# Optimization experiments

Hardware: AMD Instinct MI355X
Metric: run time of the kernel (lower is better)

Reference implementation:

```python
import jax, jax.numpy as jnp
import numpy as np

N_SP, N_SPAT = 20000, 10000
E_SS, E_BIP, E_SP = 160000, 320000, 320000
H, C = 4, 64  # GAT heads / per-head channels (hidden_channels=64, concat=False)
EPS = 1e-6


def _gat(xs, xd, row, col, ea, Ws, Wd, a_s, a_d, a_e, We, b, num_dst, heads, ch, self_loops, concat):
    # PyG GATConv with edge_dim: linear -> per-head additive attention -> softmax over incoming edges -> scatter-add
    hs = (xs @ Ws).reshape(-1, heads, ch)          # [Ns,H,C]
    hd = (xd @ Wd).reshape(-1, heads, ch)          # [Nd,H,C]
    al_s = jnp.sum(hs * a_s, -1)                   # [Ns,H]
    al_d = jnp.sum(hd * a_d, -1)                   # [Nd,H]
    if self_loops:
        # add_self_loops with fill_value='mean': loop edge_attr = mean of incoming edge_attr per node
        cnt = jax.ops.segment_sum(jnp.ones((row.shape[0],), ea.dtype), col, num_dst)
        loop_ea = jax.ops.segment_sum(ea, col, num_dst) / jnp.maximum(cnt, 1.0)[:, None]
        loops = jnp.arange(num_dst, dtype=row.dtype)
        row = jnp.concatenate([row, loops])
        col = jnp.concatenate([col, loops])
        ea = jnp.concatenate([ea, loop_ea], 0)
    he = (ea @ We).reshape(-1, heads, ch)          # [E,H,C]
    al = jax.nn.leaky_relu(al_s[row] + al_d[col] + jnp.sum(he * a_e, -1), 0.2)  # [E,H]
    m = jax.ops.segment_max(al, col, num_segments=num_dst)
    ex = jnp.exp(al - m[col])
    den = jax.ops.segment_sum(ex, col, num_segments=num_dst)
    alpha = ex / (den[col] + 1e-16)
    out = jax.ops.segment_sum(hs[row] * alpha[..., None], col, num_segments=num_dst)  # [Nd,H,C]
    out = out.reshape(num_dst, heads * ch) if concat else out.mean(1)
    return out + b


def setup_inputs() -> dict:
    key = jax.random.key(0)
    ks = iter(jax.random.split(key, 64))
    f = lambda shape: jax.random.normal(next(ks), shape, jnp.float32)
    w = lambda shape: f(shape) / np.sqrt(shape[0])
    inp = {}
    inp['species_x_mean'] = f((N_SP, 32))
    inp['species_x_std'] = jax.random.uniform(next(ks), (N_SP, 32), jnp.float32)
    inp['traits_nanmask'] = jax.random.bernoulli(next(ks), 0.4, (N_SP, 32))
    inp['species_x_gen'] = f((N_SP, 64))
    inp['species_x_phylo'] = f((N_SP, 128))
    inp['spatial_x'] = f((N_SPAT, 12))
    inp['spatial_global_data'] = f((N_SPAT, 4))
    ei = lambda e, ns, nd: jnp.stack([jax.random.randint(next(ks), (e,), 0, ns, jnp.int32),
                                      jax.random.randint(next(ks), (e,), 0, nd, jnp.int32)])
    inp['ss_edge_index'] = ei(E_SS, N_SPAT, N_SPAT)
    inp['ss_edge_attr'] = jax.random.uniform(next(ks), (E_SS, 1), jnp.float32)
    inp['bip_edge_index'] = ei(E_BIP, N_SPAT, N_SP)
    inp['bip_edge_attr'] = jax.random.uniform(next(ks), (E_BIP, 1), jnp.float32)
    inp['sp_edge_index'] = ei(E_SP, N_SP, N_SP)
    inp['sp_edge_attr'] = jax.random.uniform(next(ks), (E_SP, 1), jnp.float32)
    # GAT conv params: space_gnn (sg0, sg1), species_gnn (pg0, pg1)
    for nm, din in [('sg0', 16), ('sg1', 64), ('pg0', 128), ('pg1', 64)]:
        inp[nm + '_W'] = w((din, H * C))
        inp[nm + '_as'] = f((H, C)) * 0.1
        inp[nm + '_ad'] = f((H, C)) * 0.1
        inp[nm + '_ae'] = f((H, C)) * 0.1
        inp[nm + '_We'] = w((1, H * C))
        inp[nm + '_b'] = jnp.zeros((C,), jnp.float32)
    # bipartite GATConv: heads=1, concat=True, src dim=hidden=64, dst dim=in_gen+in_phylo=192
    inp['bp_Ws'] = w((64, 64))
    inp['bp_Wd'] = w((192, 64))
    inp['bp_as'] = f((1, 64)) * 0.1
    inp['bp_ad'] = f((1, 64)) * 0.1
    inp['bp_ae'] = f((1, 64)) * 0.1
    inp['bp_We'] = w((1, 64))
    inp['bp_b'] = jnp.zeros((64,), jnp.float32)
    inp['sl_W'] = w((288, 64))
    inp['sl_b'] = jnp.zeros((64,), jnp.float32)
    inp['fc_W'] = w((64, 64))
    inp['fc_b'] = jnp.zeros((64,), jnp.float32)
    return inp


def reference(species_x_mean, species_x_std, traits_nanmask, species_x_gen, species_x_phylo,
              spatial_x, spatial_global_data, ss_edge_index, ss_edge_attr, bip_edge_index,
              bip_edge_attr, sp_edge_index, sp_edge_attr,
              sg0_W, sg0_as, sg0_ad, sg0_ae, sg0_We, sg0_b,
              sg1_W, sg1_as, sg1_ad, sg1_ae, sg1_We, sg1_b,
              pg0_W, pg0_as, pg0_ad, pg0_ae, pg0_We, pg0_b,
              pg1_W, pg1_as, pg1_ad, pg1_ae, pg1_We, pg1_b,
              bp_Ws, bp_Wd, bp_as, bp_ad, bp_ae, bp_We, bp_b,
              sl_W, sl_b, fc_W, fc_b):
    # inference path: no trait masking -> visibility = observed mask
    vis = (~traits_nanmask).astype(jnp.float32)
    sp_in = jnp.concatenate([species_x_mean, species_x_std, vis, species_x_gen, species_x_phylo], 1)
    sp_in = jax.nn.relu(sp_in @ sl_W + sl_b)                      # [N_SP,64]
    # spatial GNN (2 GATConv layers, heads=4, concat=False, self loops)
    h = jnp.concatenate([spatial_x, spatial_global_data], 1)      # [N_SPAT,16]
    r, c = ss_edge_index[0], ss_edge_index[1]
    h = jax.nn.relu(_gat(h, h, r, c, ss_edge_attr, sg0_W, sg0_W, sg0_as, sg0_ad, sg0_ae, sg0_We, sg0_b, N_SPAT, H, C, True, False))
    h = jax.nn.relu(_gat(h, h, r, c, ss_edge_attr, sg1_W, sg1_W, sg1_as, sg1_ad, sg1_ae, sg1_We, sg1_b, N_SPAT, H, C, True, False))
    # bipartite spatial->species GATConv (heads=1, concat=True, no self loops)
    part = jnp.concatenate([species_x_gen, species_x_phylo], 1)   # [N_SP,192]
    br, bc = bip_edge_index[0], bip_edge_index[1]
    sts = jax.nn.relu(_gat(h, part, br, bc, bip_edge_attr, bp_Ws, bp_Wd, bp_as, bp_ad, bp_ae, bp_We, bp_b, N_SP, 1, 64, False, True))
    # species GNN (2 GATConv layers)
    x = jnp.concatenate([sts, sp_in], 1)                          # [N_SP,128]
    pr, pc = sp_edge_index[0], sp_edge_index[1]
    x = jax.nn.relu(_gat(x, x, pr, pc, sp_edge_attr, pg0_W, pg0_W, pg0_as, pg0_ad, pg0_ae, pg0_We, pg0_b, N_SP, H, C, True, False))
    x = jax.nn.relu(_gat(x, x, pr, pc, sp_edge_attr, pg1_W, pg1_W, pg1_as, pg1_ad, pg1_ae, pg1_We, pg1_b, N_SP, H, C, True, False))
    ms = x @ fc_W + fc_b                                          # [N_SP, 2*out]
    mean, log_std = jnp.split(ms, 2, axis=-1)
    std = jax.nn.softplus(log_std) + EPS
    return mean, std
```

## Files before the change

### kernel.cpp

```cpp
#include <hip/hip_runtime.h>
#include <hip/hip_bf16.h>

#define NSP   20000
#define NSPAT 10000
#define ESS   160000
#define EBIP  320000
#define ESP   320000

static inline int cdiv_host(long a, long b) { return (int)((a + b - 1) / b); }

__device__ __forceinline__ float wave_red_sum(float p) {
#pragma unroll
  for (int m = 32; m >= 1; m >>= 1) p += __shfl_xor(p, m, 64);
  return p;
}
__device__ __forceinline__ float bf2f(unsigned short u) {
  return __uint_as_float(((unsigned int)u) << 16);
}
__device__ __forceinline__ unsigned short f2bf(float f) {
  unsigned int u = __float_as_uint(f);
  unsigned int r = (u + 0x7FFF + ((u >> 16) & 1)) >> 16;
  return (unsigned short)r;
}

__global__ void count3_kernel(
    const int* c1, int E1, int* cp1, int* rnk1, int n1,
    const int* c2, int E2, int* cp2, int* rnk2, int n2,
    const int* c3, int E3, int* cp3, int* rnk3, int n3,
    const unsigned int* __restrict__ mask, int* __restrict__ flag) {
  int b = blockIdx.x, t = threadIdx.x;
  if (b == gridDim.x - 1) {
    if (t < 64) {
      unsigned int w0 = mask[t], w1 = mask[t + 64], w2 = mask[t + 128], w3 = mask[t + 192];
      bool ai = (w0 <= 1u) && (w1 <= 1u) && (w2 <= 1u) && (w3 <= 1u);
      auto okf = [](unsigned int w) { return w == 0u || w == 0x3f800000u; };
      bool af = okf(w0) && okf(w1) && okf(w2) && okf(w3);
      unsigned long long bi = __ballot(ai), bf = __ballot(af);
      if (t == 0) *flag = (bi == ~0ull) ? 0 : ((bf == ~0ull) ? 2 : 1);
    }
    return;
  }
  int i = b * 256 + t;
  int total = E1 + E2 + E3;
  if (i >= total) return;
  int p = (i >> 8) & 7;
  if (i < E1) {
    int d = c1[i]; rnk1[i] = atomicAdd(&cp1[p * n1 + d], 1);
  } else if (i < E1 + E2) {
    int j = i - E1;
    int d = c2[j]; rnk2[j] = atomicAdd(&cp2[p * n2 + d], 1);
  } else {
    int j = i - E1 - E2;
    int d = c3[j]; rnk3[j] = atomicAdd(&cp3[p * n3 + d], 1);
  }
}

__global__ void merge3_kernel(int* cp1, int* c1, int n1,
                              int* cp2, int* c2, int n2,
                              int* cp3, int* c3, int n3) {
  int i = blockIdx.x * blockDim.x + threadIdx.x;
  int total = n1 + n2 + n3;
  if (i >= total) return;
  int *cp, *c; int n, d;
  if (i < n1) { cp = cp1; c = c1; n = n1; d = i; }
  else if (i < n1 + n2) { cp = cp2; c = c2; n = n2; d = i - n1; }
  else { cp = cp3; c = c3; n = n3; d = i - n1 - n2; }
  int s = 0;
#pragma unroll
  for (int p = 0; p < 8; ++p) { int t = cp[p * n + d]; cp[p * n + d] = s; s += t; }
  c[d] = s;
}

__global__ __launch_bounds__(1024) void scan3_kernel(
    const int* cntA, int nA, int* ptrA,
    const int* cntB, int nB, int* ptrB,
    const int* cntC, int nC, int* ptrC) {
  const int* cnt; int n; int* ptr;
  if (blockIdx.x == 0) { cnt = cntA; n = nA; ptr = ptrA; }
  else if (blockIdx.x == 1) { cnt = cntB; n = nB; ptr = ptrB; }
  else { cnt = cntC; n = nC; ptr = ptrC; }
  __shared__ int part[1024];
  int t = threadIdx.x;
  int ch = (n + 1023) / 1024;
  int beg = t * ch, end = min(beg + ch, n);
  int s = 0;
  for (int i = beg; i < end; ++i) s += cnt[i];
  part[t] = s;
  __syncthreads();
  for (int off = 1; off < 1024; off <<= 1) {
    int v = (t >= off) ? part[t - off] : 0;
    __syncthreads();
    part[t] += v;
    __syncthreads();
  }
  int run = (t == 0) ? 0 : part[t - 1];
  for (int i = beg; i < end; ++i) { ptr[i] = run; run += cnt[i]; }
  if (t == 1023) ptr[n] = part[1023];
}

struct DoteArgs { const float* We[5]; const float* ae[5]; float* dotes; };
struct PrepArgs {
  const float* mean; const float* stdv; const void* mask; const int* flag;
  const float* sx; const float* sg; float* spc96; float* h0;
};

__global__ void scatter3x_kernel(
    const int* r1, const int* c1, const float* e1, int E1, const int* p1, const int* cp1, const int* k1, int n1, int* s1, float* a1,
    const int* r2, const int* c2, const float* e2, int E2, const int* p2, const int* cp2, const int* k2, int n2, int* s2, float* a2,
    const int* r3, const int* c3, const float* e3, int E3, const int* p3, const int* cp3, const int* k3, int n3, int* s3, float* a3,
    DoteArgs da, PrepArgs pa) {
  const int NB_SC = (ESS + EBIP + ESP + 255) / 256;
  int b = blockIdx.x, t = threadIdx.x;
  if (b < NB_SC) {
    int i = b * 256 + t;
    if (i >= E1 + E2 + E3) return;
    int p = (i >> 8) & 7;
    if (i < E1) {
      int d = c1[i];
      int pos = p1[d] + cp1[p * n1 + d] + k1[i];
      s1[pos] = r1[i]; a1[pos] = e1[i];
    } else if (i < E1 + E2) {
      int j = i - E1;
      int d = c2[j];
      int pos = p2[d] + cp2[p * n2 + d] + k2[j];
      s2[pos] = r2[j]; a2[pos] = e2[j];
    } else {
      int j = i - E1 - E2;
      int d = c3[j];
      int pos = p3[d] + cp3[p * n3 + d] + k3[j];
      s3[pos] = r3[j]; a3[pos] = e3[j];
    }
  } else if (b < NB_SC + 5) {
    int lb = b - NB_SC;
    int n = (lb == 2) ? 64 : 256;
    if (t < n) {
      float p = wave_red_sum(da.We[lb][t] * da.ae[lb][t]);
      if ((t & 63) == 0) da.dotes[lb * 4 + (t >> 6)] = p;
    }
  } else {
    const long totA = (long)NSP * 96;
    const long totB = (long)NSPAT * 16;
    long i = (long)(b - NB_SC - 5) * 256 + t;
    if (i >= totA + totB) return;
    int mode = *pa.flag;
    if (i < totA) {
      int n = (int)(i / 96), c = (int)(i % 96);
      float v;
      if (c < 32) v = pa.mean[(long)n * 32 + c];
      else if (c < 64) v = pa.stdv[(long)n * 32 + (c - 32)];
      else {
        long j = (long)n * 32 + (c - 64);
        int mv;
        if (mode == 0) mv = ((const int*)pa.mask)[j];
        else if (mode == 2) mv = (((const float*)pa.mask)[j] != 0.0f);
        else mv = (int)((const unsigned char*)pa.mask)[j];
        v = mv ? 0.f : 1.f;
      }
      pa.spc96[i] = v;
    } else {
      long k = i - totA;
      int n = (int)(k / 16), c = (int)(k % 16);
      pa.h0[k] = (c < 12) ? pa.sx[(long)n * 12 + c] : pa.sg[(long)n * 4 + (c - 12)];
    }
  }
}

struct XSrc { const float* p[5]; int w[5]; int n; };
struct PJob {
  XSrc xs; int M, K;
  const float* W; const float* bias; int mode;
  const float* a_s; const float* a_d;
  float* al_s; float* al_d;
  float* Y; float* Y2;
};
struct LeafArgs {
  const int* ss_ptr; const float* ss_cea; float* ss_lea;
  const int* pp_ptr; const float* pp_cea; float* pp_lea;
};

__device__ __forceinline__ void proj64_body(const PJob& J, int bid,
                                            float* wl, float* xl) {
  constexpr int KC = 32;
  constexpr int BR = 32;
  constexpr int KCP = 36;
  int t = threadIdx.x;
  long row0 = (long)bid * BR;
  if (row0 >= J.M) return;
  int cg = t & 15, rg = t >> 4;
  int c0 = cg * 4;

  float acc[2][4];
#pragma unroll
  for (int r = 0; r < 2; ++r)
#pragma unroll
    for (int j = 0; j < 4; ++j) acc[r][j] = 0.f;

  for (int k0 = 0; k0 < J.K; k0 += KC) {
    int seg = 0; int base = 0;
    while (k0 >= base + J.xs.w[seg]) { base += J.xs.w[seg]; ++seg; }
    const float* Xp = J.xs.p[seg];
    int stride = J.xs.w[seg];
    int kloc = k0 - base;

    __syncthreads();
    {
      const float4* ws = (const float4*)(J.W + (long)k0 * 64);
      float4* wd = (float4*)wl;
      wd[t] = ws[t];
      wd[t + 256] = ws[t + 256];
    }
// ... 51 lines not shown
        *(float4*)(J.Y + m * 64 + c0) = make_float4(
            fmaxf(v0, 0.f), fmaxf(v1, 0.f), fmaxf(v2, 0.f), fmaxf(v3, 0.f));
    } else if (J.mode == 2) {
      if (ok) {
        if (c0 < 32) {
          *(float4*)(J.Y + m * 32 + c0) = make_float4(v0, v1, v2, v3);
        } else {
          float4 o;
          o.x = fmaxf(v0, 0.f) + log1pf(__expf(-fabsf(v0))) + 1e-6f;
          o.y = fmaxf(v1, 0.f) + log1pf(__expf(-fabsf(v1))) + 1e-6f;
          o.z = fmaxf(v2, 0.f) + log1pf(__expf(-fabsf(v2))) + 1e-6f;
          o.w = fmaxf(v3, 0.f) + log1pf(__expf(-fabsf(v3))) + 1e-6f;
          *(float4*)(J.Y2 + m * 32 + (c0 - 32)) = o;
        }
      }
    } else if (ok && J.Y) {
      *(float4*)(J.Y + m * 64 + c0) = make_float4(v0, v1, v2, v3);
    }
    if (J.a_s) {
      float s = acc[r][0] * asv.x + acc[r][1] * asv.y + acc[r][2] * asv.z + acc[r][3] * asv.w;
      s += __shfl_xor(s, 1); s += __shfl_xor(s, 2);
      s += __shfl_xor(s, 4); s += __shfl_xor(s, 8);
      if (ok && cg == 0) J.al_s[m] = s;
    }
    if (J.a_d) {
      float s = acc[r][0] * adv.x + acc[r][1] * adv.y + acc[r][2] * adv.z + acc[r][3] * adv.w;
      s += __shfl_xor(s, 1); s += __shfl_xor(s, 2);
      s += __shfl_xor(s, 4); s += __shfl_xor(s, 8);
      if (ok && cg == 0) J.al_d[m] = s;
    }
  }
}

__global__ __launch_bounds__(256) void proj64x2l_kernel(PJob j0, PJob j1,
                                                        int nb0, int nb1,
                                                        LeafArgs la) {
  __shared__ float wl[32 * 64];
  __shared__ float xl[32 * 36];
  int b = blockIdx.x, t = threadIdx.x;
  if (b < nb0) {
    proj64_body(j0, b, wl, xl);
  } else if (b < nb0 + nb1) {
    proj64_body(j1, b - nb0, wl, xl);
  } else {
    int i = (b - nb0 - nb1) * 256 + t;
    if (i >= NSPAT + NSP) return;
    const int* ptr; const float* cea; float* lea; int d;
    if (i < NSPAT) { ptr = la.ss_ptr; cea = la.ss_cea; lea = la.ss_lea; d = i; }
    else { ptr = la.pp_ptr; cea = la.pp_cea; lea = la.pp_lea; d = i - NSPAT; }
    int e0 = ptr[d], e1 = ptr[d + 1];
    float s = 0.f;
    for (int e = e0; e < e1; ++e) s += cea[e];
    lea[d] = s / (float)max(e1 - e0, 1);
  }
}

__global__ __launch_bounds__(256) void proj_kernel(
    XSrc xsrc, int M, int K,
    const float* __restrict__ W,
    const float* __restrict__ a_s, const float* __restrict__ a_d,
    float* __restrict__ al_s, float* __restrict__ al_d,
    unsigned short* __restrict__ Y) {
  constexpr int KC = 32;
  constexpr int RPT = 8;
  constexpr int BR = 32;
  constexpr int KCP = 36;
  constexpr int H = 4;
  __shared__ float wl[KC * 256];
  __shared__ float xl[BR * KCP];

  int t = threadIdx.x;
  int cg = t & 63, rg = t >> 6;
  int c0 = cg * 4;
  long row0 = (long)blockIdx.x * BR;

  float acc[RPT][4];
#pragma unroll
  for (int r = 0; r < RPT; ++r)
#pragma unroll
    for (int j = 0; j < 4; ++j) acc[r][j] = 0.f;

  for (int k0 = 0; k0 < K; k0 += KC) {
    int kc = min(KC, K - k0);
    int seg = 0; int base = 0;
    while (k0 >= base + xsrc.w[seg]) { base += xsrc.w[seg]; ++seg; }
    const float* Xp = xsrc.p[seg];
    int stride = xsrc.w[seg];
    int kloc = k0 - base;

    __syncthreads();
    {
      const float4* wsrc = (const float4*)(W + (long)k0 * 256);
      float4* wdst = (float4*)wl;
      for (int i = t; i < (kc * 256) >> 2; i += 256) wdst[i] = wsrc[i];
    }
    for (int i = t; i < BR * 8; i += 256) {
      int r = i >> 3, kq = (i & 7) * 4;
      if (kq < kc) {
        long rr = row0 + r; if (rr >= M) rr = M - 1;
        float4 v = *(const float4*)(Xp + rr * stride + kloc + kq);
        *(float4*)(xl + r * KCP + kq) = v;
      }
    }
    __syncthreads();

    for (int kg = 0; kg < kc; kg += 4) {
      float4 w0 = *(const float4*)(wl + (kg + 0) * 256 + c0);
// ... 20 lines not shown
        acc[r][3] = fmaf(xv[r].z, w2.w, acc[r][3]);
        acc[r][0] = fmaf(xv[r].w, w3.x, acc[r][0]);
        acc[r][1] = fmaf(xv[r].w, w3.y, acc[r][1]);
        acc[r][2] = fmaf(xv[r].w, w3.z, acc[r][2]);
        acc[r][3] = fmaf(xv[r].w, w3.w, acc[r][3]);
      }
    }
  }

  float4 asv = *(const float4*)(a_s + c0);
  float4 adv = *(const float4*)(a_d + c0);

#pragma unroll
  for (int r = 0; r < RPT; ++r) {
    long m = row0 + (long)rg * RPT + r;
    bool ok = m < M;
    if (ok) {
      ushort4 o;
      o.x = f2bf(acc[r][0]); o.y = f2bf(acc[r][1]);
      o.z = f2bf(acc[r][2]); o.w = f2bf(acc[r][3]);
      *(ushort4*)(Y + m * 256 + c0) = o;
    }
    float s = acc[r][0] * asv.x + acc[r][1] * asv.y + acc[r][2] * asv.z + acc[r][3] * asv.w;
    s += __shfl_xor(s, 1); s += __shfl_xor(s, 2);
    s += __shfl_xor(s, 4); s += __shfl_xor(s, 8);
    if (ok && (cg & 15) == 0) al_s[m * H + (c0 >> 6)] = s;
    float d = acc[r][0] * adv.x + acc[r][1] * adv.y + acc[r][2] * adv.z + acc[r][3] * adv.w;
    d += __shfl_xor(d, 1); d += __shfl_xor(d, 2);
    d += __shfl_xor(d, 4); d += __shfl_xor(d, 8);
    if (ok && (cg & 15) == 0) al_d[m * H + (c0 >> 6)] = d;
  }
}

__device__ __forceinline__ void fma4_bf(float4& a, float al, ushort4 u) {
  a.x = fmaf(al, bf2f(u.x), a.x); a.y = fmaf(al, bf2f(u.y), a.y);
  a.z = fmaf(al, bf2f(u.z), a.z); a.w = fmaf(al, bf2f(u.w), a.w);
}
__device__ __forceinline__ void scale4(float4& a, float s) {
  a.x *= s; a.y *= s; a.z *= s; a.w *= s;
}
__device__ __forceinline__ float lrelu(float x) {
  return (x > 0.f) ? x : 0.2f * x;
}

struct OS4 { float m, d; float4 a; };
__device__ __forceinline__ void os4_init(OS4& o) {
  o.m = -INFINITY; o.d = 0.f; o.a = make_float4(0.f, 0.f, 0.f, 0.f);
}
__device__ __forceinline__ void os4_upd(OS4& o, float l, ushort4 u) {
  if (l > o.m) { float sc = __expf(o.m - l); o.d *= sc; scale4(o.a, sc); o.m = l; }
  float ex = __expf(l - o.m);
  o.d += ex; fma4_bf(o.a, ex, u);
}
__device__ __forceinline__ void os4_mrg(OS4& A, const OS4& B) {
  if (B.m == -INFINITY) return;
  if (A.m == -INFINITY) { A = B; return; }
  float M = fmaxf(A.m, B.m);
  float sA = __expf(A.m - M), sB = __expf(B.m - M);
  A.d = A.d * sA + B.d * sB;
  A.a.x = A.a.x * sA + B.a.x * sB;
  A.a.y = A.a.y * sA + B.a.y * sB;
  A.a.z = A.a.z * sA + B.a.z * sB;
  A.a.w = A.a.w * sA + B.a.w * sB;
  A.m = M;
}

template <bool SELFLOOP>
__device__ __forceinline__ float4 gat4_body(
    int n, int lane, const int* __restrict__ dptr, const int* __restrict__ csr_src,
    const float* __restrict__ csr_ea, const float* __restrict__ al_s,
    const float* __restrict__ al_d, const float* __restrict__ dote,
    const float* __restrict__ loop_ea, const unsigned short* __restrict__ hs,
    int* lds_i, float* lds_l) {
  int h = lane >> 4;
  float4 ald4 = *(const float4*)(al_d + (long)n * 4);
// ... 54 lines not shown
  float inv = 1.f / (o0.d + 1e-16f);
  scale4(o0.a, inv);
  float4 a0 = o0.a;
  a0.x += __shfl_xor(a0.x, 16); a0.y += __shfl_xor(a0.y, 16);
  a0.z += __shfl_xor(a0.z, 16); a0.w += __shfl_xor(a0.w, 16);
  a0.x += __shfl_xor(a0.x, 32); a0.y += __shfl_xor(a0.y, 32);
  a0.z += __shfl_xor(a0.z, 32); a0.w += __shfl_xor(a0.w, 32);
  return a0;
}

template <bool SELFLOOP>
__global__ __launch_bounds__(256) void gat4_fused(
    int Nd, const int* __restrict__ dptr, const int* __restrict__ csr_src,
    const float* __restrict__ csr_ea, const float* __restrict__ al_s,
    const float* __restrict__ al_d, const float* __restrict__ dote,
    const float* __restrict__ loop_ea, const unsigned short* __restrict__ hs,
    const float* __restrict__ bias, float* __restrict__ out) {
  __shared__ int li[4 * 64];
  __shared__ float ll[4 * 256];
  int wave = threadIdx.x >> 6, lane = threadIdx.x & 63;
  int n = blockIdx.x * 4 + wave;
  if (n >= Nd) return;
  float4 a0 = gat4_body<SELFLOOP>(n, lane, dptr, csr_src, csr_ea, al_s, al_d,
                                  dote, loop_ea, hs, li + wave * 64, ll + wave * 256);
  if (lane < 16) {
    float4 b = *(const float4*)(bias + lane * 4);
    float4 o;
    o.x = fmaxf(a0.x * 0.25f + b.x, 0.f);
    o.y = fmaxf(a0.y * 0.25f + b.y, 0.f);
    o.z = fmaxf(a0.z * 0.25f + b.z, 0.f);
    o.w = fmaxf(a0.w * 0.25f + b.w, 0.f);
    *(float4*)(out + (long)n * 64 + lane * 4) = o;
  }
}

__global__ __launch_bounds__(256) void gat4_fc(
    int Nd, const int* __restrict__ dptr, const int* __restrict__ csr_src,
    const float* __restrict__ csr_ea, const float* __restrict__ al_s,
    const float* __restrict__ al_d, const float* __restrict__ dote,
    const float* __restrict__ loop_ea, const unsigned short* __restrict__ hs,
    const float* __restrict__ bias, const float* __restrict__ fcW,
    const float* __restrict__ fcb, float* __restrict__ meanO,
    float* __restrict__ stdO) {
  __shared__ float Wl[64 * 64];
  __shared__ int li[4 * 64];
  __shared__ float ll[4 * 256];
  int t = threadIdx.x;
  {
    const float4* ws = (const float4*)fcW;
    float4* wd = (float4*)Wl;
    wd[t] = ws[t]; wd[t + 256] = ws[t + 256];
    wd[t + 512] = ws[t + 512]; wd[t + 768] = ws[t + 768];
  }
  __syncthreads();
  int wave = t >> 6, lane = t & 63;
  int n = blockIdx.x * 4 + wave;
  if (n >= Nd) return;
  float4 a0 = gat4_body<true>(n, lane, dptr, csr_src, csr_ea, al_s, al_d,
                              dote, loop_ea, hs, li + wave * 64, ll + wave * 256);
  float4 b = *(const float4*)(bias + (lane & 15) * 4);
  float4 o;
  o.x = fmaxf(a0.x * 0.25f + b.x, 0.f);
  o.y = fmaxf(a0.y * 0.25f + b.y, 0.f);
  o.z = fmaxf(a0.z * 0.25f + b.z, 0.f);
  o.w = fmaxf(a0.w * 0.25f + b.w, 0.f);
  float accf = 0.f;
// ... 95 lines not shown
  const int*   bip_ei  = (const int*)d_in[9];
  const float* bip_ea  = (const float*)d_in[10];
  const int*   sp_ei   = (const int*)d_in[11];
  const float* sp_ea   = (const float*)d_in[12];
  const float* sg0_W = (const float*)d_in[13]; const float* sg0_as = (const float*)d_in[14];
  const float* sg0_ad = (const float*)d_in[15]; const float* sg0_ae = (const float*)d_in[16];
  const float* sg0_We = (const float*)d_in[17]; const float* sg0_b = (const float*)d_in[18];
  const float* sg1_W = (const float*)d_in[19]; const float* sg1_as = (const float*)d_in[20];
  const float* sg1_ad = (const float*)d_in[21]; const float* sg1_ae = (const float*)d_in[22];
  const float* sg1_We = (const float*)d_in[23]; const float* sg1_b = (const float*)d_in[24];
  const float* pg0_W = (const float*)d_in[25]; const float* pg0_as = (const float*)d_in[26];
  const float* pg0_ad = (const float*)d_in[27]; const float* pg0_ae = (const float*)d_in[28];
  const float* pg0_We = (const float*)d_in[29]; const float* pg0_b = (const float*)d_in[30];
  const float* pg1_W = (const float*)d_in[31]; const float* pg1_as = (const float*)d_in[32];
  const float* pg1_ad = (const float*)d_in[33]; const float* pg1_ae = (const float*)d_in[34];
  const float* pg1_We = (const float*)d_in[35]; const float* pg1_b = (const float*)d_in[36];
  const float* bp_Ws = (const float*)d_in[37]; const float* bp_Wd = (const float*)d_in[38];
  const float* bp_as = (const float*)d_in[39]; const float* bp_ad = (const float*)d_in[40];
  const float* bp_ae = (const float*)d_in[41]; const float* bp_We = (const float*)d_in[42];
  const float* bp_b  = (const float*)d_in[43];
  const float* sl_W  = (const float*)d_in[44]; const float* sl_b  = (const float*)d_in[45];
  const float* fc_W  = (const float*)d_in[46]; const float* fc_b  = (const float*)d_in[47];

  char* wsb = (char*)d_ws;
  size_t off = 0;
  auto A = [&](size_t nbytes) -> void* {
    void* p = wsb + off;
    off += (nbytes + 255) & ~(size_t)255;
    return p;
  };
  int* ss_cp = (int*)A((size_t)8 * NSPAT * 4);
  int* bp_cp = (int*)A((size_t)8 * NSP * 4);
  int* pp_cp = (int*)A((size_t)8 * NSP * 4);
  size_t zbytes = off;
  int*   ss_cnt = (int*)A((NSPAT + 1) * 4);
  int*   bp_cnt = (int*)A((NSP + 1) * 4);
  int*   pp_cnt = (int*)A((NSP + 1) * 4);
  int*   flag  = (int*)A(4);
  float* dotes = (float*)A(5 * 4 * sizeof(float));
  float* alS   = (float*)A((size_t)NSP * 4 * 4);
  float* alD   = (float*)A((size_t)NSP * 4 * 4);
  float* alSb  = (float*)A((size_t)NSPAT * 4);
  float* alDb  = (float*)A((size_t)NSP * 4);
  float* spc96 = (float*)A((size_t)NSP * 96 * 4);
  float* sp_in = (float*)A((size_t)NSP * 64 * 4);
  float* h0    = (float*)A((size_t)NSPAT * 16 * 4);
  float* h_a   = (float*)A((size_t)NSPAT * 64 * 4);
  float* h_b   = (float*)A((size_t)NSPAT * 64 * 4);
  float* HS    = (float*)A((size_t)NSP * 256 * 4);
  float* sts   = (float*)A((size_t)NSP * 64 * 4);
  float* x1    = (float*)A((size_t)NSP * 64 * 4);
  int*   ss_ptr = (int*)A((NSPAT + 1) * 4);
  int*   ss_src = (int*)A((size_t)ESS * 4);
  float* ss_cea = (float*)A((size_t)ESS * 4);
  int*   ss_rnk = (int*)A((size_t)ESS * 4);
  float* ss_lea = (float*)A((size_t)NSPAT * 4);
  int*   bp_ptr = (int*)A((NSP + 1) * 4);
  int*   bp_src = (int*)A((size_t)EBIP * 4);
  float* bp_cea = (float*)A((size_t)EBIP * 4);
  int*   bp_rnk = (int*)A((size_t)EBIP * 4);
  int*   pp_ptr = (int*)A((NSP + 1) * 4);
  int*   pp_src = (int*)A((size_t)ESP * 4);
  float* pp_cea = (float*)A((size_t)ESP * 4);
  int*   pp_rnk = (int*)A((size_t)ESP * 4);
  float* pp_lea = (float*)A((size_t)NSP * 4);
  (void)ws_size; (void)in_sizes; (void)n_in; (void)out_size;

  const int TB = 256;
  hipMemsetAsync(wsb, 0, zbytes, stream);

  count3_kernel<<<cdiv_host(ESS + EBIP + ESP, TB) + 1, TB, 0, stream>>>(
      ss_ei + ESS, ESS, ss_cp, ss_rnk, NSPAT,
      bip_ei + EBIP, EBIP, bp_cp, bp_rnk, NSP,
      sp_ei + ESP, ESP, pp_cp, pp_rnk, NSP,
      (const unsigned int*)nanmask, flag);
  merge3_kernel<<<cdiv_host(NSPAT + NSP + NSP, TB), TB, 0, stream>>>(
      ss_cp, ss_cnt, NSPAT, bp_cp, bp_cnt, NSP, pp_cp, pp_cnt, NSP);
  scan3_kernel<<<3, 1024, 0, stream>>>(ss_cnt, NSPAT, ss_ptr, bp_cnt, NSP, bp_ptr, pp_cnt, NSP, pp_ptr);

  {
    DoteArgs da{};
    da.We[0] = sg0_We; da.ae[0] = sg0_ae;
    da.We[1] = sg1_We; da.ae[1] = sg1_ae;
    da.We[2] = bp_We;  da.ae[2] = bp_ae;
    da.We[3] = pg0_We; da.ae[3] = pg0_ae;
    da.We[4] = pg1_We; da.ae[4] = pg1_ae;
    da.dotes = dotes;
    PrepArgs pa{ sp_mean, sp_std, nanmask, flag, spat_x, spat_g, spc96, h0 };
    int nb = cdiv_host(ESS + EBIP + ESP, TB) + 5 +
             cdiv_host((long)NSP * 96 + (long)NSPAT * 16, TB);
    scatter3x_kernel<<<nb, TB, 0, stream>>>(
        ss_ei, ss_ei + ESS, ss_ea, ESS, ss_ptr, ss_cp, ss_rnk, NSPAT, ss_src, ss_cea,
        bip_ei, bip_ei + EBIP, bip_ea, EBIP, bp_ptr, bp_cp, bp_rnk, NSP, bp_src, bp_cea,
        sp_ei, sp_ei + ESP, sp_ea, ESP, pp_ptr, pp_cp, pp_rnk, NSP, pp_src, pp_cea,
        da, pa);
  }

  {
    PJob j0{}; j0.xs.p[0] = spc96; j0.xs.w[0] = 96; j0.xs.p[1] = sp_gen; j0.xs.w[1] = 64;
    j0.xs.p[2] = sp_phy; j0.xs.w[2] = 128; j0.xs.n = 3;
    j0.M = NSP; j0.K = 288; j0.W = sl_W; j0.bias = sl_b; j0.mode = 1; j0.Y = sp_in;
    PJob j1{}; j1.xs.p[0] = sp_gen; j1.xs.w[0] = 64; j1.xs.p[1] = sp_phy; j1.xs.w[1] = 128;
    j1.xs.n = 2;
    j1.M = NSP; j1.K = 192; j1.W = bp_Wd; j1.mode = 0; j1.a_d = bp_ad; j1.al_d = alDb;
    LeafArgs la{ ss_ptr, ss_cea, ss_lea, pp_ptr, pp_cea, pp_lea };
    int nb0 = cdiv_host(NSP, 32), nb1 = cdiv_host(NSP, 32);
    int nbl = cdiv_host(NSPAT + NSP, TB);
    proj64x2l_kernel<<<nb0 + nb1 + nbl, TB, 0, stream>>>(j0, j1, nb0, nb1, la);
  }

  {
    XSrc xs{}; xs.p[0] = h0; xs.w[0] = 16; xs.n = 1;
    proj_kernel<<<cdiv_host(NSPAT, 32), TB, 0, stream>>>(xs, NSPAT, 16, sg0_W,
        sg0_as, sg0_ad, alS, alD, (unsigned short*)HS);
  }
  gat4_fused<true><<<cdiv_host(NSPAT, 4), TB, 0, stream>>>(
      NSPAT, ss_ptr, ss_src, ss_cea, alS, alD, dotes + 0, ss_lea,
      (const unsigned short*)HS, sg0_b, h_a);
  {
    XSrc xs{}; xs.p[0] = h_a; xs.w[0] = 64; xs.n = 1;
    proj_kernel<<<cdiv_host(NSPAT, 32), TB, 0, stream>>>(xs, NSPAT, 64, sg1_W,
        sg1_as, sg1_ad, alS, alD, (unsigned short*)HS);
  }
  gat4_fused<true><<<cdiv_host(NSPAT, 4), TB, 0, stream>>>(
      NSPAT, ss_ptr, ss_src, ss_cea, alS, alD, dotes + 4, ss_lea,
      (const unsigned short*)HS, sg1_b, h_b);

  {
    PJob j0{}; j0.xs.p[0] = h_b; j0.xs.w[0] = 64; j0.xs.n = 1;
    j0.M = NSPAT; j0.K = 64; j0.W = bp_Ws; j0.mode = 0;
    j0.a_s = bp_as; j0.al_s = alSb; j0.Y = h_a;
    LeafArgs la{ ss_ptr, ss_cea, ss_lea, pp_ptr, pp_cea, pp_lea };
    int nb0 = cdiv_host(NSPAT, 32);
    proj64x2l_kernel<<<nb0, TB, 0, stream>>>(j0, j0, nb0, 0, la);
  }
  gat1_fused<<<cdiv_host(NSP, 4), TB, 0, stream>>>(
      NSP, bp_ptr, bp_src, bp_cea, alSb, alDb, dotes + 8, h_a, bp_b, sts);

  {
    XSrc xs{}; xs.p[0] = sts; xs.w[0] = 64; xs.p[1] = sp_in; xs.w[1] = 64; xs.n = 2;
    proj_kernel<<<cdiv_host(NSP, 32), TB, 0, stream>>>(xs, NSP, 128, pg0_W,
        pg0_as, pg0_ad, alS, alD, (unsigned short*)HS);
  }
  gat4_fused<true><<<cdiv_host(NSP, 4), TB, 0, stream>>>(
      NSP, pp_ptr, pp_src, pp_cea, alS, alD, dotes + 12, pp_lea,
      (const unsigned short*)HS, pg0_b, x1);
  {
    XSrc xs{}; xs.p[0] = x1; xs.w[0] = 64; xs.n = 1;
    proj_kernel<<<cdiv_host(NSP, 32), TB, 0, stream>>>(xs, NSP, 64, pg1_W,
        pg1_as, pg1_ad, alS, alD, (unsigned short*)HS);
  }
  gat4_fc<<<cdiv_host(NSP, 4), TB, 0, stream>>>(
      NSP, pp_ptr, pp_src, pp_cea, alS, alD, dotes + 16, pp_lea,
      (const unsigned short*)HS, pg1_b, fc_W, fc_b,
      (float*)d_out, (float*)d_out + (long)NSP * 32);
}
```

Measured before the change: 459.1 us.

## Fuse edge counting with loop-attr sums, merge scatter with projections, fold bp projection into GAT

The self-loop edge-attr means are now built with atomic adds during edge counting and divided in the merge pass, which removes the separate leaf-mean pass over the CSR. The CSR scatter now shares one launch with the first spatial projection and the two species projections. The second spatial GAT layer now also does the bipartite source projection and its attention logit, using the 64x64 weight held in shared memory. Together these cut the number of kernel launches and one intermediate round trip. The cost is float atomics, whose summation order is not fixed, and a heavier GAT epilogue.

```diff
diff --git a/kernel.cpp b/kernel.cpp
--- a/kernel.cpp
+++ b/kernel.cpp
@@ -22,53 +22,102 @@
   unsigned int r = (u + 0x7FFF + ((u >> 16) & 1)) >> 16;
   return (unsigned short)r;
 }
-
-__global__ void count3_kernel(
-    const int* c1, int E1, int* cp1, int* rnk1, int n1,
-    const int* c2, int E2, int* cp2, int* rnk2, int n2,
-    const int* c3, int E3, int* cp3, int* rnk3, int n3,
-    const unsigned int* __restrict__ mask, int* __restrict__ flag) {
+__device__ __forceinline__ float lrelu(float x) {
+  return (x > 0.f) ? x : 0.2f * x;
+}
+
+struct DoteArgs { const float* We[5]; const float* ae[5]; float* dotes; };
+struct PrepArgs {
+  const float* mean; const float* stdv; const void* mask;
+  const float* sx; const float* sg; float* spc96; float* h0;
+};
+
+__global__ void count3x_kernel(
+    const int* c1, const float* e1, int* cp1, float* les1, int* rnk1, int n1, int E1,
+    const int* c2, int* cp2, int* rnk2, int n2, int E2,
+    const int* c3, const float* e3, int* cp3, float* les3, int* rnk3, int n3, int E3,
+    DoteArgs da, PrepArgs pa) {
+  const int NB_E = (ESS + EBIP + ESP + 255) / 256;
   int b = blockIdx.x, t = threadIdx.x;
-  if (b == gridDim.x - 1) {
+  if (b < NB_E) {
+    int i = b * 256 + t;
+    if (i >= E1 + E2 + E3) return;
+    int p = (i >> 8) & 7;
+    if (i < E1) {
+      int d = c1[i];
+      rnk1[i] = atomicAdd(&cp1[p * n1 + d], 1);
+      atomicAdd(&les1[d], e1[i]);
+    } else if (i < E1 + E2) {
+      int j = i - E1;
+      int d = c2[j];
+      rnk2[j] = atomicAdd(&cp2[p * n2 + d], 1);
+    } else {
+      int j = i - E1 - E2;
+      int d = c3[j];
+      rnk3[j] = atomicAdd(&cp3[p * n3 + d], 1);
+      atomicAdd(&les3[d], e3[j]);
+    }
+  } else if (b < NB_E + 5) {
+    int lb = b - NB_E;
+    int n = (lb == 2) ? 64 : 256;
+    if (t < n) {
+      float p = wave_red_sum(da.We[lb][t] * da.ae[lb][t]);
+      if ((t & 63) == 0) da.dotes[lb * 4 + (t >> 6)] = p;
+    }
+  } else {
+    __shared__ int sflag;
     if (t < 64) {
-      unsigned int w0 = mask[t], w1 = mask[t + 64], w2 = mask[t + 128], w3 = mask[t + 192];
+      const unsigned int* mw = (const unsigned int*)pa.mask;
+      unsigned int w0 = mw[t], w1 = mw[t + 64], w2 = mw[t + 128], w3 = mw[t + 192];
       bool ai = (w0 <= 1u) && (w1 <= 1u) && (w2 <= 1u) && (w3 <= 1u);
       auto okf = [](unsigned int w) { return w == 0u || w == 0x3f800000u; };
       bool af = okf(w0) && okf(w1) && okf(w2) && okf(w3);
       unsigned long long bi = __ballot(ai), bf = __ballot(af);
-      if (t == 0) *flag = (bi == ~0ull) ? 0 : ((bf == ~0ull) ? 2 : 1);
-    }
-    return;
-  }
-  int i = b * 256 + t;
-  int total = E1 + E2 + E3;
-  if (i >= total) return;
-  int p = (i >> 8) & 7;
-  if (i < E1) {
-    int d = c1[i]; rnk1[i] = atomicAdd(&cp1[p * n1 + d], 1);
-  } else if (i < E1 + E2) {
-    int j = i - E1;
-    int d = c2[j]; rnk2[j] = atomicAdd(&cp2[p * n2 + d], 1);
-  } else {
-    int j = i - E1 - E2;
-    int d = c3[j]; rnk3[j] = atomicAdd(&cp3[p * n3 + d], 1);
-  }
-}
-
-__global__ void merge3_kernel(int* cp1, int* c1, int n1,
+      if (t == 0) sflag = (bi == ~0ull) ? 0 : ((bf == ~0ull) ? 2 : 1);
+    }
+    __syncthreads();
+    int mode = sflag;
+    const long totA = (long)NSP * 96;
+    const long totB = (long)NSPAT * 16;
+    long i = (long)(b - NB_E - 5) * 256 + t;
+    if (i >= totA + totB) return;
+    if (i < totA) {
+      int n = (int)(i / 96), c = (int)(i % 96);
+      float v;
+      if (c < 32) v = pa.mean[(long)n * 32 + c];
+      else if (c < 64) v = pa.stdv[(long)n * 32 + (c - 32)];
+      else {
+        long j = (long)n * 32 + (c - 64);
+        int mv;
+        if (mode == 0) mv = ((const int*)pa.mask)[j];
+        else if (mode == 2) mv = (((const float*)pa.mask)[j] != 0.0f);
+        else mv = (int)((const unsigned char*)pa.mask)[j];
+        v = mv ? 0.f : 1.f;
+      }
+      pa.spc96[i] = v;
+    } else {
+      long k = i - totA;
+      int n = (int)(k / 16), c = (int)(k % 16);
+      pa.h0[k] = (c < 12) ? pa.sx[(long)n * 12 + c] : pa.sg[(long)n * 4 + (c - 12)];
+    }
+  }
+}
+
+__global__ void merge3_kernel(int* cp1, int* c1, float* lea1, int n1,
                               int* cp2, int* c2, int n2,
-                              int* cp3, int* c3, int n3) {
+                              int* cp3, int* c3, float* lea3, int n3) {
   int i = blockIdx.x * blockDim.x + threadIdx.x;
   int total = n1 + n2 + n3;
   if (i >= total) return;
-  int *cp, *c; int n, d;
-  if (i < n1) { cp = cp1; c = c1; n = n1; d = i; }
-  else if (i < n1 + n2) { cp = cp2; c = c2; n = n2; d = i - n1; }
-  else { cp = cp3; c = c3; n = n3; d = i - n1 - n2; }
+  int *cp, *c; float* lea; int n, d;
+  if (i < n1) { cp = cp1; c = c1; lea = lea1; n = n1; d = i; }
+  else if (i < n1 + n2) { cp = cp2; c = c2; lea = nullptr; n = n2; d = i - n1; }
+  else { cp = cp3; c = c3; lea = lea3; n = n3; d = i - n1 - n2; }
   int s = 0;
 #pragma unroll
   for (int p = 0; p < 8; ++p) { int t = cp[p * n + d]; cp[p * n + d] = s; s += t; }
   c[d] = s;
+  if (lea) lea[d] = lea[d] / (float)max(s, 1);
 }
 
 __global__ __launch_bounds__(1024) void scan3_kernel(
@@ -98,73 +147,6 @@
   if (t == 1023) ptr[n] = part[1023];
 }
 
-struct DoteArgs { const float* We[5]; const float* ae[5]; float* dotes; };
-struct PrepArgs {
-  const float* mean; const float* stdv; const void* mask; const int* flag;
-  const float* sx; const float* sg; float* spc96; float* h0;
-};
-
-__global__ void scatter3x_kernel(
-    const int* r1, const int* c1, const float* e1, int E1, const int* p1, const int* cp1, const int* k1, int n1, int* s1, float* a1,
-    const int* r2, const int* c2, const float* e2, int E2, const int* p2, const int* cp2, const int* k2, int n2, int* s2, float* a2,
-    const int* r3, const int* c3, const float* e3, int E3, const int* p3, const int* cp3, const int* k3, int n3, int* s3, float* a3,
-    DoteArgs da, PrepArgs pa) {
-  const int NB_SC = (ESS + EBIP + ESP + 255) / 256;
-  int b = blockIdx.x, t = threadIdx.x;
-  if (b < NB_SC) {
-    int i = b * 256 + t;
-    if (i >= E1 + E2 + E3) return;
-    int p = (i >> 8) & 7;
-    if (i < E1) {
-      int d = c1[i];
-      int pos = p1[d] + cp1[p * n1 + d] + k1[i];
-      s1[pos] = r1[i]; a1[pos] = e1[i];
-    } else if (i < E1 + E2) {
-      int j = i - E1;
-      int d = c2[j];
-      int pos = p2[d] + cp2[p * n2 + d] + k2[j];
-      s2[pos] = r2[j]; a2[pos] = e2[j];
-    } else {
-      int j = i - E1 - E2;
-      int d = c3[j];
-      int pos = p3[d] + cp3[p * n3 + d] + k3[j];
-      s3[pos] = r3[j]; a3[pos] = e3[j];
-    }
-  } else if (b < NB_SC + 5) {
-    int lb = b - NB_SC;
-    int n = (lb == 2) ? 64 : 256;
-    if (t < n) {
-      float p = wave_red_sum(da.We[lb][t] * da.ae[lb][t]);
-      if ((t & 63) == 0) da.dotes[lb * 4 + (t >> 6)] = p;
-    }
-  } else {
-    const long totA = (long)NSP * 96;
-    const long totB = (long)NSPAT * 16;
-    long i = (long)(b - NB_SC - 5) * 256 + t;
-    if (i >= totA + totB) return;
-    int mode = *pa.flag;
-    if (i < totA) {
-      int n = (int)(i / 96), c = (int)(i % 96);
-      float v;
-      if (c < 32) v = pa.mean[(long)n * 32 + c];
-      else if (c < 64) v = pa.stdv[(long)n * 32 + (c - 32)];
-      else {
-        long j = (long)n * 32 + (c - 64);
-        int mv;
-        if (mode == 0) mv = ((const int*)pa.mask)[j];
-        else if (mode == 2) mv = (((const float*)pa.mask)[j] != 0.0f);
-        else mv = (int)((const unsigned char*)pa.mask)[j];
-        v = mv ? 0.f : 1.f;
-      }
-      pa.spc96[i] = v;
-    } else {
-      long k = i - totA;
-      int n = (int)(k / 16), c = (int)(k % 16);
-      pa.h0[k] = (c < 12) ? pa.sx[(long)n * 12 + c] : pa.sg[(long)n * 4 + (c - 12)];
-    }
-  }
-}
-
 struct XSrc { const float* p[5]; int w[5]; int n; };
 struct PJob {
   XSrc xs; int M, K;
@@ -172,10 +154,6 @@
   const float* a_s; const float* a_d;
   float* al_s; float* al_d;
   float* Y; float* Y2;
-};
-struct LeafArgs {
-  const int* ss_ptr; const float* ss_cea; float* ss_lea;
-  const int* pp_ptr; const float* pp_cea; float* pp_lea;
 };
 
 __device__ __forceinline__ void proj64_body(const PJob& J, int bid,
@@ -293,47 +271,22 @@
   }
 }
 
-__global__ __launch_bounds__(256) void proj64x2l_kernel(PJob j0, PJob j1,
-                                                        int nb0, int nb1,
-                                                        LeafArgs la) {
-  __shared__ float wl[32 * 64];
-  __shared__ float xl[32 * 36];
-  int b = blockIdx.x, t = threadIdx.x;
-  if (b < nb0) {
-    proj64_body(j0, b, wl, xl);
-  } else if (b < nb0 + nb1) {
-    proj64_body(j1, b - nb0, wl, xl);
-  } else {
-    int i = (b - nb0 - nb1) * 256 + t;
-    if (i >= NSPAT + NSP) return;
-    const int* ptr; const float* cea; float* lea; int d;
-    if (i < NSPAT) { ptr = la.ss_ptr; cea = la.ss_cea; lea = la.ss_lea; d = i; }
-    else { ptr = la.pp_ptr; cea = la.pp_cea; lea = la.pp_lea; d = i - NSPAT; }
-    int e0 = ptr[d], e1 = ptr[d + 1];
-    float s = 0.f;
-    for (int e = e0; e < e1; ++e) s += cea[e];
-    lea[d] = s / (float)max(e1 - e0, 1);
-  }
-}
-
-__global__ __launch_bounds__(256) void proj_kernel(
-    XSrc xsrc, int M, int K,
+__device__ __forceinline__ void proj256_body(
+    const XSrc& xsrc, int M, int K,
     const float* __restrict__ W,
     const float* __restrict__ a_s, const float* __restrict__ a_d,
     float* __restrict__ al_s, float* __restrict__ al_d,
-    unsigned short* __restrict__ Y) {
+    unsigned short* __restrict__ Y, int bid, float* wl, float* xl) {
   constexpr int KC = 32;
   constexpr int RPT = 8;
   constexpr int BR = 32;
   constexpr int KCP = 36;
   constexpr int H = 4;
-  __shared__ float wl[KC * 256];
-  __shared__ float xl[BR * KCP];
-
   int t = threadIdx.x;
   int cg = t & 63, rg = t >> 6;
   int c0 = cg * 4;
-  long row0 = (long)blockIdx.x * BR;
+  long row0 = (long)bid * BR;
+  if (row0 >= M) return;
 
   float acc[RPT][4];
 #pragma unroll
@@ -420,15 +373,62 @@
   }
 }
 
+__global__ __launch_bounds__(256) void proj_kernel(
+    XSrc xsrc, int M, int K,
+    const float* __restrict__ W,
+    const float* __restrict__ a_s, const float* __restrict__ a_d,
+    float* __restrict__ al_s, float* __restrict__ al_d,
+    unsigned short* __restrict__ Y) {
+  __shared__ float wl[32 * 256];
+  __shared__ float xl[32 * 36];
+  proj256_body(xsrc, M, K, W, a_s, a_d, al_s, al_d, Y, blockIdx.x, wl, xl);
+}
+
+__global__ __launch_bounds__(256) void scatterproj_kernel(
+    const int* r1, const int* c1, const float* e1, int E1, const int* p1, const int* cp1, const int* k1, int n1, int* s1, float* a1,
+    const int* r2, const int* c2, const float* e2, int E2, const int* p2, const int* cp2, const int* k2, int n2, int* s2, float* a2,
+    const int* r3, const int* c3, const float* e3, int E3, const int* p3, const int* cp3, const int* k3, int n3, int* s3, float* a3,
+    PJob jsl, PJob jbp,
+    XSrc xs0, int M0, int K0, const float* W0, const float* as0, const float* ad0,
+    float* alS0, float* alD0, unsigned short* Y0, int nb0, int nbsl) {
+  __shared__ float wl[32 * 256];
+  __shared__ float xl[32 * 36];
+  const int NB_SC = (ESS + EBIP + ESP + 255) / 256;
+  int b = blockIdx.x, t = threadIdx.x;
+  if (b < NB_SC) {
+    int i = b * 256 + t;
+    if (i >= E1 + E2 + E3) return;
+    int p = (i >> 8) & 7;
+    if (i < E1) {
+      int d = c1[i];
+      int pos = p1[d] + cp1[p * n1 + d] + k1[i];
+      s1[pos] = r1[i]; a1[pos] = e1[i];
+    } else if (i < E1 + E2) {
+      int j = i - E1;
+      int d = c2[j];
+      int pos = p2[d] + cp2[p * n2 + d] + k2[j];
+      s2[pos] = r2[j]; a2[pos] = e2[j];
+    } else {
+      int j = i - E1 - E2;
+      int d = c3[j];
+      int pos = p3[d] + cp3[p * n3 + d] + k3[j];
+      s3[pos] = r3[j]; a3[pos] = e3[j];
+    }
+  } else if (b < NB_SC + nb0) {
+    proj256_body(xs0, M0, K0, W0, as0, ad0, alS0, alD0, Y0, b - NB_SC, wl, xl);
+  } else if (b < NB_SC + nb0 + nbsl) {
+    proj64_body(jsl, b - NB_SC - nb0, wl, xl);
+  } else {
+    proj64_body(jbp, b - NB_SC - nb0 - nbsl, wl, xl);
+  }
+}
+
 __device__ __forceinline__ void fma4_bf(float4& a, float al, ushort4 u) {
   a.x = fmaf(al, bf2f(u.x), a.x); a.y = fmaf(al, bf2f(u.y), a.y);
   a.z = fmaf(al, bf2f(u.z), a.z); a.w = fmaf(al, bf2f(u.w), a.w);
 }
 __device__ __forceinline__ void scale4(float4& a, float s) {
   a.x *= s; a.y *= s; a.z *= s; a.w *= s;
-}
-__device__ __forceinline__ float lrelu(float x) {
-  return (x > 0.f) ? x : 0.2f * x;
 }
 
 struct OS4 { float m, d; float4 a; };
@@ -549,6 +549,51 @@
     o.w = fmaxf(a0.w * 0.25f + b.w, 0.f);
     *(float4*)(out + (long)n * 64 + lane * 4) = o;
   }
+}
+
+__global__ __launch_bounds__(256) void gat4_bp(
+    int Nd, const int* __restrict__ dptr, const int* __restrict__ csr_src,
+    const float* __restrict__ csr_ea, const float* __restrict__ al_s,
+    const float* __restrict__ al_d, const float* __restrict__ dote,
+    const float* __restrict__ loop_ea, const unsigned short* __restrict__ hs,
+    const float* __restrict__ bias, const float* __restrict__ bpW,
+    const float* __restrict__ bp_as, float* __restrict__ hsrc,
+    float* __restrict__ alSb) {
+  __shared__ float Wl[64 * 64];
+  __shared__ int li[4 * 64];
+  __shared__ float ll[4 * 256];
+  int t = threadIdx.x;
+  {
+    const float4* ws = (const float4*)bpW;
+    float4* wd = (float4*)Wl;
+    wd[t] = ws[t]; wd[t + 256] = ws[t + 256];
+    wd[t + 512] = ws[t + 512]; wd[t + 768] = ws[t + 768];
+  }
+  __syncthreads();
+  int wave = t >> 6, lane = t & 63;
+  int n = blockIdx.x * 4 + wave;
+  if (n >= Nd) return;
+  float4 a0 = gat4_body<true>(n, lane, dptr, csr_src, csr_ea, al_s, al_d,
+                              dote, loop_ea, hs, li + wave * 64, ll + wave * 256);
+  float4 b = *(const float4*)(bias + (lane & 15) * 4);
+  float4 o;
+  o.x = fmaxf(a0.x * 0.25f + b.x, 0.f);
+  o.y = fmaxf(a0.y * 0.25f + b.y, 0.f);
+  o.z = fmaxf(a0.z * 0.25f + b.z, 0.f);
+  o.w = fmaxf(a0.w * 0.25f + b.w, 0.f);
+  float accf = 0.f;
+#pragma unroll
+  for (int q = 0; q < 16; ++q) {
+    float vx = __shfl(o.x, q), vy = __shfl(o.y, q);
+    float vz = __shfl(o.z, q), vw = __shfl(o.w, q);
+    accf = fmaf(vx, Wl[(4 * q + 0) * 64 + lane], accf);
+    accf = fmaf(vy, Wl[(4 * q + 1) * 64 + lane], accf);
+    accf = fmaf(vz, Wl[(4 * q + 2) * 64 + lane], accf);
+    accf = fmaf(vw, Wl[(4 * q + 3) * 64 + lane], accf);
+  }
+  hsrc[(long)n * 64 + lane] = accf;
+  float s = wave_red_sum(accf * bp_as[lane]);
+  if (lane == 0) alSb[n] = s;
 }
 
 __global__ __launch_bounds__(256) void gat4_fc(
@@ -710,11 +755,12 @@
   int* ss_cp = (int*)A((size_t)8 * NSPAT * 4);
   int* bp_cp = (int*)A((size_t)8 * NSP * 4);
   int* pp_cp = (int*)A((size_t)8 * NSP * 4);
+  float* ss_lea = (float*)A((size_t)NSPAT * 4);
+  float* pp_lea = (float*)A((size_t)NSP * 4);
   size_t zbytes = off;
   int*   ss_cnt = (int*)A((NSPAT + 1) * 4);
   int*   bp_cnt = (int*)A((NSP + 1) * 4);
   int*   pp_cnt = (int*)A((NSP + 1) * 4);
-  int*   flag  = (int*)A(4);
   float* dotes = (float*)A(5 * 4 * sizeof(float));
   float* alS   = (float*)A((size_t)NSP * 4 * 4);
   float* alD   = (float*)A((size_t)NSP * 4 * 4);
@@ -724,7 +770,6 @@
   float* sp_in = (float*)A((size_t)NSP * 64 * 4);
   float* h0    = (float*)A((size_t)NSPAT * 16 * 4);
   float* h_a   = (float*)A((size_t)NSPAT * 64 * 4);
-  float* h_b   = (float*)A((size_t)NSPAT * 64 * 4);
   float* HS    = (float*)A((size_t)NSP * 256 * 4);
   float* sts   = (float*)A((size_t)NSP * 64 * 4);
   float* x1    = (float*)A((size_t)NSP * 64 * 4);
@@ -732,7 +777,6 @@
   int*   ss_src = (int*)A((size_t)ESS * 4);
   float* ss_cea = (float*)A((size_t)ESS * 4);
   int*   ss_rnk = (int*)A((size_t)ESS * 4);
-  float* ss_lea = (float*)A((size_t)NSPAT * 4);
   int*   bp_ptr = (int*)A((NSP + 1) * 4);
   int*   bp_src = (int*)A((size_t)EBIP * 4);
   float* bp_cea = (float*)A((size_t)EBIP * 4);
@@ -741,20 +785,10 @@
   int*   pp_src = (int*)A((size_t)ESP * 4);
   float* pp_cea = (float*)A((size_t)ESP * 4);
   int*   pp_rnk = (int*)A((size_t)ESP * 4);
-  float* pp_lea = (float*)A((size_t)NSP * 4);
   (void)ws_size; (void)in_sizes; (void)n_in; (void)out_size;
 
   const int TB = 256;
   hipMemsetAsync(wsb, 0, zbytes, stream);
-
-  count3_kernel<<<cdiv_host(ESS + EBIP + ESP, TB) + 1, TB, 0, stream>>>(
-      ss_ei + ESS, ESS, ss_cp, ss_rnk, NSPAT,
-      bip_ei + EBIP, EBIP, bp_cp, bp_rnk, NSP,
-      sp_ei + ESP, ESP, pp_cp, pp_rnk, NSP,
-      (const unsigned int*)nanmask, flag);
-  merge3_kernel<<<cdiv_host(NSPAT + NSP + NSP, TB), TB, 0, stream>>>(
-      ss_cp, ss_cnt, NSPAT, bp_cp, bp_cnt, NSP, pp_cp, pp_cnt, NSP);
-  scan3_kernel<<<3, 1024, 0, stream>>>(ss_cnt, NSPAT, ss_ptr, bp_cnt, NSP, bp_ptr, pp_cnt, NSP, pp_ptr);
 
   {
     DoteArgs da{};
@@ -764,34 +798,40 @@
     da.We[3] = pg0_We; da.ae[3] = pg0_ae;
     da.We[4] = pg1_We; da.ae[4] = pg1_ae;
     da.dotes = dotes;
-    PrepArgs pa{ sp_mean, sp_std, nanmask, flag, spat_x, spat_g, spc96, h0 };
+    PrepArgs pa{ sp_mean, sp_std, nanmask, spat_x, spat_g, spc96, h0 };
     int nb = cdiv_host(ESS + EBIP + ESP, TB) + 5 +
              cdiv_host((long)NSP * 96 + (long)NSPAT * 16, TB);
-    scatter3x_kernel<<<nb, TB, 0, stream>>>(
+    count3x_kernel<<<nb, TB, 0, stream>>>(
+        ss_ei + ESS, ss_ea, ss_cp, ss_lea, ss_rnk, NSPAT, ESS,
+        bip_ei + EBIP, bp_cp, bp_rnk, NSP, EBIP,
+        sp_ei + ESP, sp_ea, pp_cp, pp_lea, pp_rnk, NSP, ESP,
+        da, pa);
+  }
+  merge3_kernel<<<cdiv_host(NSPAT + NSP + NSP, TB), TB, 0, stream>>>(
+      ss_cp, ss_cnt, ss_lea, NSPAT, bp_cp, bp_cnt, NSP, pp_cp, pp_cnt, pp_lea, NSP);
+  scan3_kernel<<<3, 1024, 0, stream>>>(ss_cnt, NSPAT, ss_ptr, bp_cnt, NSP, bp_ptr, pp_cnt, NSP, pp_ptr);
+
+  {
+    PJob jsl{}; jsl.xs.p[0] = spc96; jsl.xs.w[0] = 96; jsl.xs.p[1] = sp_gen; jsl.xs.w[1] = 64;
+    jsl.xs.p[2] = sp_phy; jsl.xs.w[2] = 128; jsl.xs.n = 3;
+    jsl.M = NSP; jsl.K = 288; jsl.W = sl_W; jsl.bias = sl_b; jsl.mode = 1; jsl.Y = sp_in;
+    PJob jbp{}; jbp.xs.p[0] = sp_gen; jbp.xs.w[0] = 64; jbp.xs.p[1] = sp_phy; jbp.xs.w[1] = 128;
+    jbp.xs.n = 2;
+    jbp.M = NSP; jbp.K = 192; jbp.W = bp_Wd; jbp.mode = 0; jbp.a_d = bp_ad; jbp.al_d = alDb;
+    XSrc xs0{}; xs0.p[0] = h0; xs0.w[0] = 16; xs0.n = 1;
+    int nb_sc = cdiv_host(ESS + EBIP + ESP, TB);
+    int nb0 = cdiv_host(NSPAT, 32);
+    int nbsl = cdiv_host(NSP, 32);
+    int nbbp = cdiv_host(NSP, 32);
+    scatterproj_kernel<<<nb_sc + nb0 + nbsl + nbbp, TB, 0, stream>>>(
         ss_ei, ss_ei + ESS, ss_ea, ESS, ss_ptr, ss_cp, ss_rnk, NSPAT, ss_src, ss_cea,
         bip_ei, bip_ei + EBIP, bip_ea, EBIP, bp_ptr, bp_cp, bp_rnk, NSP, bp_src, bp_cea,
         sp_ei, sp_ei + ESP, sp_ea, ESP, pp_ptr, pp_cp, pp_rnk, NSP, pp_src, pp_cea,
-        da, pa);
-  }
-
-  {
-    PJob j0{}; j0.xs.p[0] = spc96; j0.xs.w[0] = 96; j0.xs.p[1] = sp_gen; j0.xs.w[1] = 64;
-    j0.xs.p[2] = sp_phy; j0.xs.w[2] = 128; j0.xs.n = 3;
-    j0.M = NSP; j0.K = 288; j0.W = sl_W; j0.bias = sl_b; j0.mode = 1; j0.Y = sp_in;
-    PJob j1{}; j1.xs.p[0] = sp_gen; j1.xs.w[0] = 64; j1.xs.p[1] = sp_phy; j1.xs.w[1] = 128;
-    j1.xs.n = 2;
-    j1.M = NSP; j1.K = 192; j1.W = bp_Wd; j1.mode = 0; j1.a_d = bp_ad; j1.al_d = alDb;
-    LeafArgs la{ ss_ptr, ss_cea, ss_lea, pp_ptr, pp_cea, pp_lea };
-    int nb0 = cdiv_host(NSP, 32), nb1 = cdiv_host(NSP, 32);
-    int nbl = cdiv_host(NSPAT + NSP, TB);
-    proj64x2l_kernel<<<nb0 + nb1 + nbl, TB, 0, stream>>>(j0, j1, nb0, nb1, la);
-  }
-
-  {
-    XSrc xs{}; xs.p[0] = h0; xs.w[0] = 16; xs.n = 1;
-    proj_kernel<<<cdiv_host(NSPAT, 32), TB, 0, stream>>>(xs, NSPAT, 16, sg0_W,
-        sg0_as, sg0_ad, alS, alD, (unsigned short*)HS);
-  }
+        jsl, jbp,
+        xs0, NSPAT, 16, sg0_W, sg0_as, sg0_ad, alS, alD, (unsigned short*)HS,
+        nb0, nbsl);
+  }
+
   gat4_fused<true><<<cdiv_host(NSPAT, 4), TB, 0, stream>>>(
       NSPAT, ss_ptr, ss_src, ss_cea, alS, alD, dotes + 0, ss_lea,
       (const unsigned short*)HS, sg0_b, h_a);
@@ -800,18 +840,10 @@
     proj_kernel<<<cdiv_host(NSPAT, 32), TB, 0, stream>>>(xs, NSPAT, 64, sg1_W,
         sg1_as, sg1_ad, alS, alD, (unsigned short*)HS);
   }
-  gat4_fused<true><<<cdiv_host(NSPAT, 4), TB, 0, stream>>>(
+  gat4_bp<<<cdiv_host(NSPAT, 4), TB, 0, stream>>>(
       NSPAT, ss_ptr, ss_src, ss_cea, alS, alD, dotes + 4, ss_lea,
-      (const unsigned short*)HS, sg1_b, h_b);
-
-  {
-    PJob j0{}; j0.xs.p[0] = h_b; j0.xs.w[0] = 64; j0.xs.n = 1;
-    j0.M = NSPAT; j0.K = 64; j0.W = bp_Ws; j0.mode = 0;
-    j0.a_s = bp_as; j0.al_s = alSb; j0.Y = h_a;
-    LeafArgs la{ ss_ptr, ss_cea, ss_lea, pp_ptr, pp_cea, pp_lea };
-    int nb0 = cdiv_host(NSPAT, 32);
-    proj64x2l_kernel<<<nb0, TB, 0, stream>>>(j0, j0, nb0, 0, la);
-  }
+      (const unsigned short*)HS, sg1_b, bp_Ws, bp_as, h_a, alSb);
+
   gat1_fused<<<cdiv_host(NSP, 4), TB, 0, stream>>>(
       NSP, bp_ptr, bp_src, bp_cea, alSb, alDb, dotes + 8, h_a, bp_b, sts);
 
```

New measurement: 478.0 us. 4.1% more time.
